# Optimization experiments

Measured on AMD Instinct MI355X. Metric: run time of the kernel, lower is better.

The kernel has to match this reference:

```python
import jax, jax.numpy as jnp
import numpy as np

B, S, D, V, L = 8, 8192, 768, 64, 26  # batch, seq, hidden, symbol vocab, labels


def setup_inputs() -> dict:
    key = jax.random.key(0)
    k1, k2, k3 = jax.random.split(key, 3)
    hidden_states = jax.random.normal(k1, (B, S, D), dtype=jnp.float32)
    input_ids = jax.random.randint(k2, (B, S), 0, V, dtype=jnp.int32)
    W = jax.random.normal(k3, (L, D), dtype=jnp.float32) * 0.02
    b = jnp.zeros((L,), dtype=jnp.float32)
    return {"hidden_states": hidden_states, "W": W, "b": b, "input_ids": input_ids}


def reference(hidden_states, W, b, input_ids):
    # Per-batch, per-symbol mean pooling of hidden states, then linear classify.
    # Dense/padded equivalent of the torch per-symbol boolean-mask loop:
    # row (batch_b, symbol_v) = classifier(mean of hidden_states[b] where input_ids[b]==v),
    # masked to 0 for symbol 0 and for symbols absent in the sequence.
    Bv, Sv, Dv = hidden_states.shape
    seg = (input_ids + jnp.arange(Bv, dtype=input_ids.dtype)[:, None] * V).reshape(-1)
    flat_h = hidden_states.reshape(-1, Dv)
    sums = jax.ops.segment_sum(flat_h, seg, num_segments=Bv * V)            # [B*V, D]
    counts = jax.ops.segment_sum(
        jnp.ones((Bv * Sv,), dtype=hidden_states.dtype), seg, num_segments=Bv * V
    )                                                                        # [B*V]
    means = sums / jnp.maximum(counts, 1.0)[:, None]
    logits = means @ W.T + b                                                 # [B*V, L]
    present = (counts > 0) & ((jnp.arange(Bv * V) % V) > 0)                  # exclude symbol 0
    logits = jnp.where(present[:, None], logits, 0.0)
    return logits.reshape(Bv, V, -1)
```

## Files before the change

### kernel.cpp

```cpp
#include <hip/hip_runtime.h>

#define B_ 8
#define S_ 8192
#define D_ 768
#define V_ 64
#define L_ 26

typedef __attribute__((ext_vector_type(8))) short short8;
typedef __attribute__((ext_vector_type(4))) float floatx4;

#define TOKS 256
#define SLICES (S_ / TOKS)
#define NSL  48

__global__ __launch_bounds__(256, 4) void pool_mfma_kernel(
    const float* __restrict__ h, const int* __restrict__ ids,
    float* __restrict__ part, unsigned int* __restrict__ cntpart)
{
    __shared__ unsigned int cnt[V_];

    const int tid  = threadIdx.x;
    const int lane = tid & 63;
    const int wave = tid >> 6;
    const int nl   = lane & 15;
    const int quad = lane >> 4;

    const int b     = blockIdx.z;
    const int slice = blockIdx.x;
    const int k0    = slice * TOKS;
    const int n0    = blockIdx.y * (4 * NSL) + wave * NSL;

    const int*   idrow = ids + b * S_ + k0;
    const float* hrow  = h + ((size_t)b * S_ + k0) * D_ + n0;

    if (blockIdx.y == 0) {
        if (tid < V_) cnt[tid] = 0u;
        __syncthreads();
        if (tid < TOKS / 4) {
            const int4 q = ((const int4*)idrow)[tid];
            atomicAdd(&cnt[q.x], 1u); atomicAdd(&cnt[q.y], 1u);
            atomicAdd(&cnt[q.z], 1u); atomicAdd(&cnt[q.w], 1u);
        }
        __syncthreads();
        if (tid < V_) cntpart[(slice * B_ + b) * V_ + tid] = cnt[tid];
    }

    floatx4 acc[4][3];
    #pragma unroll
    for (int mt = 0; mt < 4; ++mt)
        #pragma unroll
        for (int nt = 0; nt < 3; ++nt) acc[mt][nt] = (floatx4)0.f;

    for (int ks = 0; ks < TOKS; ks += 32) {
        const int kb = ks + quad * 8;
        const int4* ip = (const int4*)(idrow + kb);
        const int4 i0 = ip[0], i1 = ip[1];
        const int idv[8] = {i0.x, i0.y, i0.z, i0.w, i1.x, i1.y, i1.z, i1.w};

        float f[3][8];
        #pragma unroll
        for (int nt = 0; nt < 3; ++nt) {
            const float* bp = hrow + (size_t)kb * D_ + nt * 16 + nl;
            #pragma unroll
            for (int j = 0; j < 8; ++j) f[nt][j] = bp[(size_t)j * D_];
        }

        short8 afrag[4];
        #pragma unroll
        for (int j = 0; j < 8; ++j) {
            const int id  = idv[j];
            const short e = ((id & 15) == nl) ? (short)0x3F80 : (short)0;
            const int hi4 = id >> 4;
            #pragma unroll
            for (int mt = 0; mt < 4; ++mt)
                afrag[mt][j] = (hi4 == mt) ? e : (short)0;
        }

        #pragma unroll
        for (int nt = 0; nt < 3; ++nt) {
            short8 bhi, blo;
            #pragma unroll
            for (int j = 0; j < 8; ++j) {
                const unsigned u = __builtin_bit_cast(unsigned, f[nt][j]);
                bhi[j] = (short)(u >> 16);
                const float hif = __builtin_bit_cast(float, u & 0xFFFF0000u);
                const float lof = f[nt][j] - hif;
                blo[j] = (short)(__builtin_bit_cast(unsigned, lof) >> 16);
            }
            #pragma unroll
            for (int mt = 0; mt < 4; ++mt) {
                acc[mt][nt] = __builtin_amdgcn_mfma_f32_16x16x32_bf16(
                    afrag[mt], bhi, acc[mt][nt], 0, 0, 0);
                acc[mt][nt] = __builtin_amdgcn_mfma_f32_16x16x32_bf16(
                    afrag[mt], blo, acc[mt][nt], 0, 0, 0);
            }
        }
    }

    float* pbase = part + ((size_t)(slice * B_ + b) * V_) * D_;
    #pragma unroll
    for (int mt = 0; mt < 4; ++mt)
        #pragma unroll
        for (int nt = 0; nt < 3; ++nt)
            #pragma unroll
            for (int r = 0; r < 4; ++r) {
                const int v = mt * 16 + quad * 4 + r;
                const int d = n0 + nt * 16 + nl;
                pbase[(size_t)v * D_ + d] = acc[mt][nt][r];
            }
}

__global__ __launch_bounds__(256) void reduce_finalize_kernel(
    const float* __restrict__ part, const unsigned int* __restrict__ cntpart,
    const float* __restrict__ Wm, const float* __restrict__ bias,
    float* __restrict__ out)
{
    __shared__ float mean[D_];
    __shared__ unsigned int scnt;

    const int tid = threadIdx.x;
    const int bv  = blockIdx.x;
    const int b   = bv >> 6;
    const int v   = bv & (V_ - 1);

    if (tid == 0) scnt = 0u;
    __syncthreads();
    if (tid < SLICES)
        atomicAdd(&scnt, cntpart[(tid * B_ + b) * V_ + v]);

    float s[3];
    #pragma unroll
    for (int j = 0; j < 3; ++j) {
        const int d = tid + j * 256;
        float a = 0.f;
        #pragma unroll
        for (int sl = 0; sl < SLICES; ++sl)
            a += part[((size_t)(sl * B_ + b) * V_ + v) * D_ + d];
        s[j] = a;
    }
    __syncthreads();
    const unsigned int c = scnt;
    const float inv = 1.f / (float)(c > 1u ? c : 1u);
    #pragma unroll
    for (int j = 0; j < 3; ++j) mean[tid + j * 256] = s[j] * inv;
    __syncthreads();

    const bool present = (c > 0u) && (v > 0);
    const int lane = tid & 63;
    const int wave = tid >> 6;
    for (int l = wave; l < L_; l += 4) {
        const float* wrow = Wm + l * D_;
        float p = 0.f;
        #pragma unroll
        for (int j = 0; j < 12; ++j) {
            const int d = lane + 64 * j;
            p += mean[d] * wrow[d];
        }
        #pragma unroll
        for (int off = 32; off > 0; off >>= 1) p += __shfl_down(p, off);
        if (lane == 0) out[bv * L_ + l] = present ? (p + bias[l]) : 0.f;
    }
}

extern "C" void kernel_launch(void* const* d_in, const int* in_sizes, int n_in,
                              void* d_out, int out_size, void* d_ws, size_t ws_size,
                              hipStream_t stream) {
    const float* h    = (const float*)d_in[0];
    const float* Wm   = (const float*)d_in[1];
    const float* bias = (const float*)d_in[2];
    const int*   ids  = (const int*)d_in[3];
    float* out = (float*)d_out;

    float* part = (float*)d_ws;
    unsigned int* cntpart =
        (unsigned int*)(part + (size_t)SLICES * B_ * V_ * D_);

    dim3 grid1(SLICES, D_ / (4 * NSL), B_);
    pool_mfma_kernel<<<grid1, 256, 0, stream>>>(h, ids, part, cntpart);

    reduce_finalize_kernel<<<B_ * V_, 256, 0, stream>>>(
        part, cntpart, Wm, bias, out);
}
```

Baseline: 306.4 us.

## Double-buffer token loads, double slice length, vectorize partial reduction

```diff
diff --git a/kernel.cpp b/kernel.cpp
--- a/kernel.cpp
+++ b/kernel.cpp
@@ -9,11 +9,64 @@
 typedef __attribute__((ext_vector_type(8))) short short8;
 typedef __attribute__((ext_vector_type(4))) float floatx4;
 
-#define TOKS 256
+#define TOKS 512
 #define SLICES (S_ / TOKS)
 #define NSL  48
-
-__global__ __launch_bounds__(256, 4) void pool_mfma_kernel(
+#define KSTEPS (TOKS / 32)
+
+__device__ __forceinline__ void load_kstep(
+    const float* __restrict__ hrow, const int* __restrict__ idrow,
+    int kk, int quad, int nl, float (&f)[3][8], int4& i0, int4& i1)
+{
+    const int kb = kk * 32 + quad * 8;
+    const int4* ip = (const int4*)(idrow + kb);
+    i0 = ip[0]; i1 = ip[1];
+    #pragma unroll
+    for (int nt = 0; nt < 3; ++nt) {
+        const float* bp = hrow + (size_t)kb * D_ + nt * 16 + nl;
+        #pragma unroll
+        for (int j = 0; j < 8; ++j) f[nt][j] = bp[(size_t)j * D_];
+    }
+}
+
+__device__ __forceinline__ void compute_kstep(
+    const float (&f)[3][8], int4 i0, int4 i1, int nl, floatx4 (&acc)[4][3])
+{
+    const int idv[8] = {i0.x, i0.y, i0.z, i0.w, i1.x, i1.y, i1.z, i1.w};
+
+    short8 afrag[4];
+    #pragma unroll
+    for (int j = 0; j < 8; ++j) {
+        const int id  = idv[j];
+        const short e = ((id & 15) == nl) ? (short)0x3F80 : (short)0;
+        const int hi4 = id >> 4;
+        #pragma unroll
+        for (int mt = 0; mt < 4; ++mt)
+            afrag[mt][j] = (hi4 == mt) ? e : (short)0;
+    }
+
+    #pragma unroll
+    for (int nt = 0; nt < 3; ++nt) {
+        short8 bhi, blo;
+        #pragma unroll
+        for (int j = 0; j < 8; ++j) {
+            const unsigned u = __builtin_bit_cast(unsigned, f[nt][j]);
+            bhi[j] = (short)(u >> 16);
+            const float hif = __builtin_bit_cast(float, u & 0xFFFF0000u);
+            const float lof = f[nt][j] - hif;
+            blo[j] = (short)(__builtin_bit_cast(unsigned, lof) >> 16);
+        }
+        #pragma unroll
+        for (int mt = 0; mt < 4; ++mt) {
+            acc[mt][nt] = __builtin_amdgcn_mfma_f32_16x16x32_bf16(
+                afrag[mt], bhi, acc[mt][nt], 0, 0, 0);
+            acc[mt][nt] = __builtin_amdgcn_mfma_f32_16x16x32_bf16(
+                afrag[mt], blo, acc[mt][nt], 0, 0, 0);
+        }
+    }
+}
+
+__global__ __launch_bounds__(256, 2) void pool_mfma_kernel(
     const float* __restrict__ h, const int* __restrict__ ids,
     float* __restrict__ part, unsigned int* __restrict__ cntpart)
 {
@@ -51,50 +104,16 @@
         #pragma unroll
         for (int nt = 0; nt < 3; ++nt) acc[mt][nt] = (floatx4)0.f;
 
-    for (int ks = 0; ks < TOKS; ks += 32) {
-        const int kb = ks + quad * 8;
-        const int4* ip = (const int4*)(idrow + kb);
-        const int4 i0 = ip[0], i1 = ip[1];
-        const int idv[8] = {i0.x, i0.y, i0.z, i0.w, i1.x, i1.y, i1.z, i1.w};
-
-        float f[3][8];
-        #pragma unroll
-        for (int nt = 0; nt < 3; ++nt) {
-            const float* bp = hrow + (size_t)kb * D_ + nt * 16 + nl;
-            #pragma unroll
-            for (int j = 0; j < 8; ++j) f[nt][j] = bp[(size_t)j * D_];
-        }
-
-        short8 afrag[4];
-        #pragma unroll
-        for (int j = 0; j < 8; ++j) {
-            const int id  = idv[j];
-            const short e = ((id & 15) == nl) ? (short)0x3F80 : (short)0;
-            const int hi4 = id >> 4;
-            #pragma unroll
-            for (int mt = 0; mt < 4; ++mt)
-                afrag[mt][j] = (hi4 == mt) ? e : (short)0;
-        }
-
-        #pragma unroll
-        for (int nt = 0; nt < 3; ++nt) {
-            short8 bhi, blo;
-            #pragma unroll
-            for (int j = 0; j < 8; ++j) {
-                const unsigned u = __builtin_bit_cast(unsigned, f[nt][j]);
-                bhi[j] = (short)(u >> 16);
-                const float hif = __builtin_bit_cast(float, u & 0xFFFF0000u);
-                const float lof = f[nt][j] - hif;
-                blo[j] = (short)(__builtin_bit_cast(unsigned, lof) >> 16);
-            }
-            #pragma unroll
-            for (int mt = 0; mt < 4; ++mt) {
-                acc[mt][nt] = __builtin_amdgcn_mfma_f32_16x16x32_bf16(
-                    afrag[mt], bhi, acc[mt][nt], 0, 0, 0);
-                acc[mt][nt] = __builtin_amdgcn_mfma_f32_16x16x32_bf16(
-                    afrag[mt], blo, acc[mt][nt], 0, 0, 0);
-            }
-        }
+    float fA[3][8], fB[3][8];
+    int4 iA0, iA1, iB0, iB1;
+    load_kstep(hrow, idrow, 0, quad, nl, fA, iA0, iA1);
+    #pragma unroll
+    for (int ks = 0; ks < KSTEPS; ks += 2) {
+        load_kstep(hrow, idrow, ks + 1, quad, nl, fB, iB0, iB1);
+        compute_kstep(fA, iA0, iA1, nl, acc);
+        if (ks + 2 < KSTEPS)
+            load_kstep(hrow, idrow, ks + 2, quad, nl, fA, iA0, iA1);
+        compute_kstep(fB, iB0, iB1, nl, acc);
     }
 
     float* pbase = part + ((size_t)(slice * B_ + b) * V_) * D_;
@@ -128,21 +147,22 @@
     if (tid < SLICES)
         atomicAdd(&scnt, cntpart[(tid * B_ + b) * V_ + v]);
 
-    float s[3];
-    #pragma unroll
-    for (int j = 0; j < 3; ++j) {
-        const int d = tid + j * 256;
-        float a = 0.f;
-        #pragma unroll
-        for (int sl = 0; sl < SLICES; ++sl)
-            a += part[((size_t)(sl * B_ + b) * V_ + v) * D_ + d];
-        s[j] = a;
+    floatx4 s4 = (floatx4)0.f;
+    if (tid < D_ / 4) {
+        #pragma unroll
+        for (int sl = 0; sl < SLICES; ++sl) {
+            const floatx4 p4 = *(const floatx4*)
+                &part[((size_t)(sl * B_ + b) * V_ + v) * D_ + 4 * tid];
+            s4 += p4;
+        }
     }
     __syncthreads();
     const unsigned int c = scnt;
     const float inv = 1.f / (float)(c > 1u ? c : 1u);
-    #pragma unroll
-    for (int j = 0; j < 3; ++j) mean[tid + j * 256] = s[j] * inv;
+    if (tid < D_ / 4) {
+        #pragma unroll
+        for (int x = 0; x < 4; ++x) mean[4 * tid + x] = s4[x] * inv;
+    }
     __syncthreads();
 
     const bool present = (c > 0u) && (v > 0);
```

Measured after the change: 296.5 us. 3.2% less time.
